# Kernel optimization log

Measured on AMD Instinct MI355X. Metric: run time of the kernel, lower is better.

## Reference

```python
import jax, jax.numpy as jnp
import numpy as np

L_LEVELS = 10
LEVEL_DIM = 4
BASE_RES = 16
T_HASH = 2 ** 21
DEG_VIEW = 4
DENSITY_BIAS = -1.0
RGB_PADDING = 0.001
RES = (BASE_RES * 2 ** np.arange(L_LEVELS)).astype(np.float32)  # 16..8192
CORNERS = np.array([[(i >> 2) & 1, (i >> 1) & 1, i & 1] for i in range(8)], np.int32)  # [8,3]
P1 = jnp.uint32(2654435761)
P2 = jnp.uint32(805459861)


def hash_grid_encode(pts, embeddings):
    """pts [N,3] in [-1,1]; embeddings [L,T,D] -> [N,L,D] trilinear hash-grid features."""
    x01 = (pts + 1.0) * 0.5  # [N,3] in [0,1]

    def level(emb, r):
        pos = x01 * r - 0.5  # align_corners=False style
        p0 = jnp.floor(pos)
        frac = pos - p0  # [N,3]
        coords = (p0.astype(jnp.int32)[:, None, :] + CORNERS).astype(jnp.uint32)  # [N,8,3]
        h = coords[..., 0] ^ (coords[..., 1] * P1) ^ (coords[..., 2] * P2)
        idx = (h & jnp.uint32(T_HASH - 1)).astype(jnp.int32)  # [N,8]
        w = jnp.prod(jnp.where(CORNERS == 1, frac[:, None, :], 1.0 - frac[:, None, :]), axis=-1)  # [N,8]
        vals = emb[idx]  # [N,8,D]
        return jnp.einsum('ncd,nc->nd', vals, w)

    feats = jax.vmap(level)(embeddings, jnp.asarray(RES))  # [L,N,D]
    return jnp.moveaxis(feats, 0, 1)  # [N,L,D]


def pos_enc(d, min_deg=0, max_deg=DEG_VIEW):
    scales = 2.0 ** jnp.arange(min_deg, max_deg, dtype=jnp.float32)
    xb = (d[..., None, :] * scales[:, None]).reshape(*d.shape[:-1], -1)  # [...,3*deg]
    four = jnp.sin(jnp.concatenate([xb, xb + 0.5 * jnp.pi], axis=-1))
    return jnp.concatenate([d, four], axis=-1)  # [..., 3 + 6*deg] = 27


def setup_inputs() -> dict:
    key = jax.random.key(0)
    ks = jax.random.split(key, 10)
    B, S, n = 1024, 32, 6
    means = jax.random.uniform(ks[0], (B, S, n, 3), minval=-1.0, maxval=1.0)
    stds = jax.random.uniform(ks[1], (B, S, n), minval=0.001, maxval=0.05)
    vd = jax.random.normal(ks[2], (B, 3))
    viewdirs = vd / jnp.linalg.norm(vd, axis=-1, keepdims=True)
    embeddings = jax.random.normal(ks[3], (L_LEVELS, T_HASH, LEVEL_DIM)) * 0.1

    def lin(k, i, o):
        return jax.random.normal(k, (i, o)) * (1.0 / np.sqrt(i))

    return {
        'rand': 0,
        'means': means, 'stds': stds, 'viewdirs': viewdirs, 'embeddings': embeddings,
        'Wd0': lin(ks[4], 40, 64), 'bd0': jnp.zeros(64),
        'Wd1': lin(ks[5], 64, 256), 'bd1': jnp.zeros(256),
        'Wv0': lin(ks[6], 283, 256), 'bv0': jnp.zeros(256),
        'Wv1': lin(ks[7], 539, 256), 'bv1': jnp.zeros(256),
        'Wr': lin(ks[8], 256, 3), 'br': jnp.zeros(3),
    }


def reference(rand, means, stds, viewdirs, embeddings, Wd0, bd0, Wd1, bd1,
              Wv0, bv0, Wv1, bv1, Wr, br):
    B, S, n = means.shape[:3]
    # --- predict_density ---
    feats = hash_grid_encode(means.reshape(-1, 3), embeddings)
    feats = feats.reshape(B, S, n, L_LEVELS, LEVEL_DIM)
    gs = jnp.asarray(RES)
    # erf re-weighting by per-level grid size (ZipNeRF anti-aliasing)
    w = jax.lax.erf(1.0 / jnp.clip(jnp.sqrt(8.0 * stds[..., None] ** 2 * gs ** 2), 1e-10))  # [B,S,n,L]
    feat = (feats * w[..., None]).mean(axis=-3).reshape(B, S, L_LEVELS * LEVEL_DIM)  # mean over multisamples n
    h = jax.nn.relu(feat @ Wd0 + bd0)
    x = h @ Wd1 + bd1  # [B,S,256] bottleneck
    density = jax.nn.softplus(x[..., 0] + DENSITY_BIAS)
    # --- view-dependent rgb branch ---
    dir_enc = pos_enc(viewdirs)  # [B,27]
    de = jnp.broadcast_to(dir_enc[:, None, :], (B, S, dir_enc.shape[-1]))
    x_in = jnp.concatenate([x, de], axis=-1)  # [B,S,283]
    h = jax.nn.relu(x_in @ Wv0 + bv0)
    h = jnp.concatenate([h, x_in], axis=-1)  # skip connection at layer 0 -> [B,S,539]
    h = jax.nn.relu(h @ Wv1 + bv1)
    rgb = jax.nn.sigmoid(h @ Wr + br)  # rgb_premultiplier=1, rgb_bias=0
    rgb = rgb * (1.0 + 2.0 * RGB_PADDING) - RGB_PADDING
    return density, rgb
```

## Files before the change

### kernel.cpp

```cpp
#include <hip/hip_runtime.h>

#define HASH_T    2097152u
#define HASH_MASK 2097151u
#define PRIME1 2654435761u
#define PRIME2 805459861u

typedef __attribute__((ext_vector_type(8))) short bf16x8;
typedef __attribute__((ext_vector_type(4))) float f32x4;
typedef __attribute__((ext_vector_type(4))) unsigned short us4;

__device__ __forceinline__ unsigned short bf16_hi(float x){
    unsigned u = __float_as_uint(x);
    return (unsigned short)((u + 0x7FFFu + ((u >> 16) & 1u)) >> 16);
}
__device__ __forceinline__ float bf16f(unsigned short h){
    return __uint_as_float((unsigned)h << 16);
}
__device__ __forceinline__ void split2(float x, unsigned short& h, unsigned short& l){
    h = bf16_hi(x);
    l = bf16_hi(x - bf16f(h));
}

__global__ __launch_bounds__(256) void pack_weights_kernel(
    const float* __restrict__ Wd0, const float* __restrict__ Wd1,
    const float* __restrict__ Wv0, const float* __restrict__ Wv1,
    unsigned short* __restrict__ pk)
{
    int tid = blockIdx.x * 256 + threadIdx.x;
    if (tid >= 424 * 512) return;
    int pair = tid >> 9;
    int li   = tid & 511;
    int lane = li >> 3, j = li & 7;
    int kq = ((lane >> 4) << 3) + j;
    int cl = lane & 15;
    float w;
    if (pair < 8) {
        int idx = pair; int kt = idx >> 2, ct = idx & 3;
        int k = kt * 32 + kq, c = ct * 16 + cl;
        w = (k < 40) ? Wd0[k * 64 + c] : 0.0f;
    } else if (pair < 40) {
        int idx = pair - 8; int kt = idx >> 4, ct = idx & 15;
        int k = kt * 32 + kq, c = ct * 16 + cl;
        w = Wd1[k * 256 + c];
    } else if (pair < 168) {
        int idx = pair - 40; int kt = idx >> 4, ct = idx & 15;
        int k = kt * 32 + kq, c = ct * 16 + cl;
        w = Wv0[k * 256 + c];
    } else {
        int idx = pair - 168;
        int kt = idx >> 4, ct = idx & 15;
        int k = kt * 32 + kq, c = ct * 16 + cl;
        int refr = (k < 256) ? (k + 256) : (k - 256);
        w = Wv1[refr * 256 + c];
    }
    unsigned short h, l; split2(w, h, l);
    pk[(size_t)pair * 1024 + li]       = h;
    pk[(size_t)pair * 1024 + 512 + li] = l;
}

__global__ __launch_bounds__(256) void hash_encode_kernel(
    const float* __restrict__ means, const float* __restrict__ stds,
    const float* __restrict__ emb, float* __restrict__ feat, int NS)
{
    int gid = blockIdx.x * 256 + threadIdx.x;
    if (gid >= NS * 10) return;
    int l = gid / NS;
    int s = gid - l * NS;
    float r = (float)(16 << l);
    const float* __restrict__ embL = emb + (size_t)l * (size_t)HASH_T * 4u;

    float a0 = 0.f, a1 = 0.f, a2 = 0.f, a3 = 0.f;
    #pragma unroll
    for (int n = 0; n < 6; ++n) {
        const float* mp = means + ((size_t)s * 6 + n) * 3;
        float sd = stds[(size_t)s * 6 + n];
        float px = (mp[0] + 1.0f) * 0.5f * r - 0.5f;
        float py = (mp[1] + 1.0f) * 0.5f * r - 0.5f;
        float pz = (mp[2] + 1.0f) * 0.5f * r - 0.5f;
        float fx = floorf(px), fy = floorf(py), fz = floorf(pz);
        float rx = px - fx, ry = py - fy, rz = pz - fz;
        int ix = (int)fx, iy = (int)fy, iz = (int)fz;
        unsigned hx[2] = { (unsigned)ix,          (unsigned)(ix + 1) };
        unsigned hy[2] = { (unsigned)iy * PRIME1, (unsigned)(iy + 1) * PRIME1 };
        unsigned hz[2] = { (unsigned)iz * PRIME2, (unsigned)(iz + 1) * PRIME2 };
        float wx[2] = { 1.0f - rx, rx };
        float wy[2] = { 1.0f - ry, ry };
        float wz[2] = { 1.0f - rz, rz };
        float t8 = 8.0f * (sd * sd) * (r * r);
        float wl = erff(1.0f / fmaxf(sqrtf(t8), 1e-10f));
        float v0 = 0.f, v1 = 0.f, v2 = 0.f, v3 = 0.f;
        #pragma unroll
        for (int c = 0; c < 8; ++c) {
            int bx = (c >> 2) & 1, by = (c >> 1) & 1, bz = c & 1;
            unsigned idx = (hx[bx] ^ hy[by] ^ hz[bz]) & HASH_MASK;
            const float4 e = *reinterpret_cast<const float4*>(embL + (size_t)idx * 4u);
            float w = wx[bx] * wy[by] * wz[bz];
            v0 += w * e.x; v1 += w * e.y; v2 += w * e.z; v3 += w * e.w;
        }
        a0 += wl * v0; a1 += wl * v1; a2 += wl * v2; a3 += wl * v3;
    }
    const float inv6 = 1.0f / 6.0f;
    float4 o; o.x = a0 * inv6; o.y = a1 * inv6; o.z = a2 * inv6; o.w = a3 * inv6;
    *reinterpret_cast<float4*>(feat + (size_t)s * 40 + l * 4) = o;
}

template<int KT, int NC>
__device__ __forceinline__ void gemm_layer(
    const unsigned short* __restrict__ pkBase, int NCT, int ct0, int kOff,
    const unsigned short (*Ahi)[584], const unsigned short (*Alo)[584],
    int lane, f32x4 acc[NC][2])
{
    const int r = lane & 15;
    const int kg = (lane >> 4) * 8;
    for (int kt = 0; kt < KT; ++kt) {
        const int ke = kOff + kt * 32 + kg;
        bf16x8 bh[2], bl[2];
        #pragma unroll
        for (int st = 0; st < 2; ++st) {
            bh[st] = *reinterpret_cast<const bf16x8*>(&Ahi[st * 16 + r][ke]);
            bl[st] = *reinterpret_cast<const bf16x8*>(&Alo[st * 16 + r][ke]);
        }
        #pragma unroll
        for (int ci = 0; ci < NC; ++ci) {
            const unsigned short* pf = pkBase + (size_t)(kt * NCT + ct0 + ci) * 1024 + lane * 8;
            bf16x8 ah = *reinterpret_cast<const bf16x8*>(pf);
            bf16x8 al = *reinterpret_cast<const bf16x8*>(pf + 512);
            #pragma unroll
            for (int st = 0; st < 2; ++st) {
                acc[ci][st] = __builtin_amdgcn_mfma_f32_16x16x32_bf16(ah, bh[st], acc[ci][st], 0, 0, 0);
                acc[ci][st] = __builtin_amdgcn_mfma_f32_16x16x32_bf16(ah, bl[st], acc[ci][st], 0, 0, 0);
                acc[ci][st] = __builtin_amdgcn_mfma_f32_16x16x32_bf16(al, bh[st], acc[ci][st], 0, 0, 0);
            }
        }
    }
}

template<int NC, bool RELU>
__device__ __forceinline__ void epilogue_store(
    f32x4 acc[NC][2], int ct0, int lane, const float* bias, int outOff,
    unsigned short (*Ahi)[584], unsigned short (*Alo)[584])
{
    const int r = lane & 15, g = lane >> 4;
    #pragma unroll
    for (int ci = 0; ci < NC; ++ci) {
        const int c0 = (ct0 + ci) * 16 + g * 4;
        const float4 bb = *reinterpret_cast<const float4*>(&bias[c0]);
        #pragma unroll
        for (int st = 0; st < 2; ++st) {
            const int s = st * 16 + r;
            float v[4] = { acc[ci][st][0] + bb.x, acc[ci][st][1] + bb.y,
                           acc[ci][st][2] + bb.z, acc[ci][st][3] + bb.w };
            us4 H, L;
            #pragma unroll
            for (int q = 0; q < 4; ++q) {
                float vv = RELU ? fmaxf(v[q], 0.0f) : v[q];
                unsigned short h, l; split2(vv, h, l);
                H[q] = h; L[q] = l;
            }
            *reinterpret_cast<us4*>(&Ahi[s][outOff + c0]) = H;
            *reinterpret_cast<us4*>(&Alo[s][outOff + c0]) = L;
        }
    }
}

__global__ __launch_bounds__(256, 2) void mlp_mfma_kernel(
    const float* __restrict__ feat, const float* __restrict__ vdirs,
    const unsigned short* __restrict__ pk,
    const float* __restrict__ bd0, const float* __restrict__ bd1,
    const float* __restrict__ Wv0, const float* __restrict__ bv0,
    const float* __restrict__ Wv1, const float* __restrict__ bv1,
    const float* __restrict__ Wr,  const float* __restrict__ br,
    float* __restrict__ outD, float* __restrict__ outRGB)
{
    __shared__ __align__(16) unsigned short sAhi[32][584];
    __shared__ __align__(16) unsigned short sAlo[32][584];
    __shared__ float sDe[32];
    __shared__ float sDv0[256];
    __shared__ float sDv1[256];
    __shared__ float sRed[32][8][3];

    const int t = threadIdx.x;
    const int lane = t & 63;
    const int w = t >> 6;
    const int b = blockIdx.x;
    const int base = b * 32;

    {
        int s = t >> 3, kg = t & 7;
        float v[8];
        if (kg < 5) {
            const float* fp = feat + (size_t)(base + s) * 40 + kg * 8;
            #pragma unroll
            for (int q = 0; q < 8; ++q) v[q] = fp[q];
        } else {
            #pragma unroll
            for (int q = 0; q < 8; ++q) v[q] = 0.0f;
        }
        us4 H0, H1, L0v, L1v;
        #pragma unroll
        for (int q = 0; q < 4; ++q) {
            unsigned short h, l;
            split2(v[q], h, l);       H0[q] = h; L0v[q] = l;
            split2(v[q + 4], h, l);   H1[q] = h; L1v[q] = l;
        }
        *reinterpret_cast<us4*>(&sAhi[s][kg * 8])     = H0;
        *reinterpret_cast<us4*>(&sAhi[s][kg * 8 + 4]) = H1;
        *reinterpret_cast<us4*>(&sAlo[s][kg * 8])     = L0v;
        *reinterpret_cast<us4*>(&sAlo[s][kg * 8 + 4]) = L1v;
    }
    if (t < 27) {
        float d0 = vdirs[b * 3 + 0], d1 = vdirs[b * 3 + 1], d2 = vdirs[b * 3 + 2];
        float val;
        if (t < 3) val = (t == 0) ? d0 : ((t == 1) ? d1 : d2);
        else {
            int u = t - 3, half = u / 12, jk = u % 12;
            int j = jk / 3, k = jk % 3;
            float dk = (k == 0) ? d0 : ((k == 1) ? d1 : d2);
            float xb = dk * (float)(1 << j);
            val = sinf(half ? (xb + 1.57079632679489662f) : xb);
        }
        sDe[t] = val;
    }
    __syncthreads();

    {
        int c = t;
        float a0 = bv0[c], a1 = bv1[c];
        #pragma unroll
        for (int k = 0; k < 27; ++k) {
            float dv = sDe[k];
            a0 += dv * Wv0[(256 + k) * 256 + c];
            a1 += dv * Wv1[(512 + k) * 256 + c];
        }
        sDv0[c] = a0; sDv1[c] = a1;
    }

    {
        f32x4 acc[1][2] = {};
        gemm_layer<2, 1>(pk, 4, w, 0, sAhi, sAlo, lane, acc);
        __syncthreads();
        epilogue_store<1, true>(acc, w, lane, bd0, 0, sAhi, sAlo);
    }
    __syncthreads();

    {
        f32x4 acc[4][2] = {};
        gemm_layer<2, 4>(pk + 8192, 16, w * 4, 0, sAhi, sAlo, lane, acc);
        if (w == 0 && (lane >> 4) == 0) {
            #pragma unroll
            for (int st = 0; st < 2; ++st) {
                float x0 = acc[0][st][0] + bd1[0];
                int s = st * 16 + (lane & 15);
                float vv = x0 - 1.0f;
                outD[base + s] = fmaxf(vv, 0.0f) + log1pf(expf(-fabsf(vv)));
            }
        }
        epilogue_store<4, false>(acc, w * 4, lane, bd1, 64, sAhi, sAlo);
    }
    __syncthreads();

    {
        f32x4 acc[4][2] = {};
        gemm_layer<8, 4>(pk + 40960, 16, w * 4, 64, sAhi, sAlo, lane, acc);
        epilogue_store<4, true>(acc, w * 4, lane, sDv0, 320, sAhi, sAlo);
    }
    __syncthreads();

    {
        f32x4 acc[4][2] = {};
        gemm_layer<16, 4>(pk + 172032, 16, w * 4, 64, sAhi, sAlo, lane, acc);
        __syncthreads();
        epilogue_store<4, true>(acc, w * 4, lane, sDv1, 0, sAhi, sAlo);
    }
    __syncthreads();

    {
        int s = t & 31, jj = t >> 5;
        float p0 = 0.f, p1 = 0.f, p2 = 0.f;
        int k0 = jj * 32;
        #pragma unroll 2
        for (int q = 0; q < 4; ++q) {
            us4 vh[2], vl[2];
            *reinterpret_cast<uint4*>(vh) = *reinterpret_cast<const uint4*>(&sAhi[s][k0 + q * 8]);
            *reinterpret_cast<uint4*>(vl) = *reinterpret_cast<const uint4*>(&sAlo[s][k0 + q * 8]);
            #pragma unroll
            for (int e = 0; e < 8; ++e) {
                int k = k0 + q * 8 + e;
                float hv = bf16f(((const unsigned short*)vh)[e]) + bf16f(((const unsigned short*)vl)[e]);
                p0 += hv * Wr[k * 3 + 0];
                p1 += hv * Wr[k * 3 + 1];
                p2 += hv * Wr[k * 3 + 2];
            }
        }
        sRed[s][jj][0] = p0; sRed[s][jj][1] = p1; sRed[s][jj][2] = p2;
    }
    __syncthreads();
    if (t < 96) {
        int s = t & 31, ch = t >> 5;
        float a = br[ch];
        #pragma unroll
        for (int j = 0; j < 8; ++j) a += sRed[s][j][ch];
        float sg = 1.0f / (1.0f + expf(-a));
        outRGB[(size_t)(base + s) * 3 + ch] = sg * 1.002f - 0.001f;
    }
}

extern "C" void kernel_launch(void* const* d_in, const int* in_sizes, int n_in,
                              void* d_out, int out_size, void* d_ws, size_t ws_size,
                              hipStream_t stream) {
    const float* means = (const float*)d_in[1];
    const float* stds_ = (const float*)d_in[2];
    const float* vdirs = (const float*)d_in[3];
    const float* emb   = (const float*)d_in[4];
    const float* Wd0 = (const float*)d_in[5];
    const float* bd0 = (const float*)d_in[6];
    const float* Wd1 = (const float*)d_in[7];
    const float* bd1 = (const float*)d_in[8];
    const float* Wv0 = (const float*)d_in[9];
    const float* bv0 = (const float*)d_in[10];
    const float* Wv1 = (const float*)d_in[11];
    const float* bv1 = (const float*)d_in[12];
    const float* Wr  = (const float*)d_in[13];
    const float* br  = (const float*)d_in[14];

    const int B  = in_sizes[3] / 3;
    const int NS = B * 32;

    float* feat = (float*)d_ws;
    unsigned short* pk = (unsigned short*)((char*)d_ws + (size_t)NS * 40 * 4);

    hipLaunchKernelGGL(pack_weights_kernel, dim3((424 * 512 + 255) / 256), dim3(256), 0, stream,
                       Wd0, Wd1, Wv0, Wv1, pk);

    int total = NS * 10;
    hipLaunchKernelGGL(hash_encode_kernel, dim3((total + 255) / 256), dim3(256), 0, stream,
                       means, stds_, emb, feat, NS);

    float* outD   = (float*)d_out;
    float* outRGB = outD + NS;
    hipLaunchKernelGGL(mlp_mfma_kernel, dim3(B), dim3(256), 0, stream,
                       feat, vdirs, pk, bd0, bd1, Wv0, bv0, Wv1, bv1, Wr, br,
                       outD, outRGB);
}
```

Measured before the change: 229.9 us.

## Remap hash encoding to wave-per-sample lanes and widen MLP tiles to 64 rows

The hash encoder now assigns one wavefront per group of samples, with each lane handling one multisample-corner pair and reducing across the wave with shuffles. Previously each thread walked all 48 gathers for one sample and level. The MLP kernel now processes 64 rows per 512-thread block and prefetches the next k-tile of packed weights into registers. It also vectorizes feature loads and replaces the shared-memory RGB reduction with shuffles. The goal is more memory-level parallelism in the gathers and more reuse of each weight fragment. The cost is more shuffle work per level, lanes left idle (n>=6), and higher register and LDS use per block.

```diff
diff --git a/kernel.cpp b/kernel.cpp
--- a/kernel.cpp
+++ b/kernel.cpp
@@ -58,95 +58,121 @@
     pk[(size_t)pair * 1024 + 512 + li] = l;
 }
 
-__global__ __launch_bounds__(256) void hash_encode_kernel(
+__global__ __launch_bounds__(256, 4) void hash_encode_wave(
     const float* __restrict__ means, const float* __restrict__ stds,
     const float* __restrict__ emb, float* __restrict__ feat, int NS)
 {
-    int gid = blockIdx.x * 256 + threadIdx.x;
-    if (gid >= NS * 10) return;
-    int l = gid / NS;
-    int s = gid - l * NS;
-    float r = (float)(16 << l);
-    const float* __restrict__ embL = emb + (size_t)l * (size_t)HASH_T * 4u;
-
-    float a0 = 0.f, a1 = 0.f, a2 = 0.f, a3 = 0.f;
-    #pragma unroll
-    for (int n = 0; n < 6; ++n) {
-        const float* mp = means + ((size_t)s * 6 + n) * 3;
-        float sd = stds[(size_t)s * 6 + n];
-        float px = (mp[0] + 1.0f) * 0.5f * r - 0.5f;
-        float py = (mp[1] + 1.0f) * 0.5f * r - 0.5f;
-        float pz = (mp[2] + 1.0f) * 0.5f * r - 0.5f;
-        float fx = floorf(px), fy = floorf(py), fz = floorf(pz);
-        float rx = px - fx, ry = py - fy, rz = pz - fz;
-        int ix = (int)fx, iy = (int)fy, iz = (int)fz;
-        unsigned hx[2] = { (unsigned)ix,          (unsigned)(ix + 1) };
-        unsigned hy[2] = { (unsigned)iy * PRIME1, (unsigned)(iy + 1) * PRIME1 };
-        unsigned hz[2] = { (unsigned)iz * PRIME2, (unsigned)(iz + 1) * PRIME2 };
-        float wx[2] = { 1.0f - rx, rx };
-        float wy[2] = { 1.0f - ry, ry };
-        float wz[2] = { 1.0f - rz, rz };
-        float t8 = 8.0f * (sd * sd) * (r * r);
-        float wl = erff(1.0f / fmaxf(sqrtf(t8), 1e-10f));
-        float v0 = 0.f, v1 = 0.f, v2 = 0.f, v3 = 0.f;
-        #pragma unroll
-        for (int c = 0; c < 8; ++c) {
-            int bx = (c >> 2) & 1, by = (c >> 1) & 1, bz = c & 1;
-            unsigned idx = (hx[bx] ^ hy[by] ^ hz[bz]) & HASH_MASK;
-            const float4 e = *reinterpret_cast<const float4*>(embL + (size_t)idx * 4u);
-            float w = wx[bx] * wy[by] * wz[bz];
-            v0 += w * e.x; v1 += w * e.y; v2 += w * e.z; v3 += w * e.w;
-        }
-        a0 += wl * v0; a1 += wl * v1; a2 += wl * v2; a3 += wl * v3;
-    }
+    const int lane = threadIdx.x & 63;
+    const int gwave = (blockIdx.x * 256 + threadIdx.x) >> 6;
+    const int n = lane >> 3;
+    const int c = lane & 7;
+    const int bx = (c >> 2) & 1, by = (c >> 1) & 1, bz = c & 1;
+    const bool act = (n < 6);
     const float inv6 = 1.0f / 6.0f;
-    float4 o; o.x = a0 * inv6; o.y = a1 * inv6; o.z = a2 * inv6; o.w = a3 * inv6;
-    *reinterpret_cast<float4*>(feat + (size_t)s * 40 + l * 4) = o;
+
+    int s0 = gwave * 4;
+    for (int si = 0; si < 4; ++si) {
+        int s = s0 + si;
+        if (s >= NS) return;
+        float mx = 0.f, my = 0.f, mz = 0.f, sd = 1.0f;
+        if (act) {
+            const float* mp = means + ((size_t)s * 6 + n) * 3;
+            mx = mp[0]; my = mp[1]; mz = mp[2];
+            sd = stds[(size_t)s * 6 + n];
+        }
+        float sd2_8 = 8.0f * sd * sd;
+        #pragma unroll 2
+        for (int l = 0; l < 10; ++l) {
+            float r = (float)(16 << l);
+            float px = (mx + 1.0f) * 0.5f * r - 0.5f;
+            float py = (my + 1.0f) * 0.5f * r - 0.5f;
+            float pz = (mz + 1.0f) * 0.5f * r - 0.5f;
+            float fx = floorf(px), fy = floorf(py), fz = floorf(pz);
+            float rx = px - fx, ry = py - fy, rz = pz - fz;
+            int ix = (int)fx + bx, iy = (int)fy + by, iz = (int)fz + bz;
+            unsigned h = (unsigned)ix ^ ((unsigned)iy * PRIME1) ^ ((unsigned)iz * PRIME2);
+            unsigned idx = h & HASH_MASK;
+            float wx = bx ? rx : 1.0f - rx;
+            float wy = by ? ry : 1.0f - ry;
+            float wz = bz ? rz : 1.0f - rz;
+            float wl = erff(1.0f / fmaxf(sqrtf(sd2_8 * r * r), 1e-10f));
+            float w = act ? (wx * wy * wz) * wl : 0.0f;
+            const float4 e = *reinterpret_cast<const float4*>(
+                emb + ((size_t)l * HASH_T + idx) * 4u);
+            float a0 = w * e.x, a1 = w * e.y, a2 = w * e.z, a3 = w * e.w;
+            #pragma unroll
+            for (int m = 1; m < 64; m <<= 1) {
+                a0 += __shfl_xor(a0, m);
+                a1 += __shfl_xor(a1, m);
+                a2 += __shfl_xor(a2, m);
+                a3 += __shfl_xor(a3, m);
+            }
+            if (lane == 0) {
+                float4 o; o.x = a0 * inv6; o.y = a1 * inv6; o.z = a2 * inv6; o.w = a3 * inv6;
+                *reinterpret_cast<float4*>(feat + (size_t)s * 40 + l * 4) = o;
+            }
+        }
+    }
 }
 
 template<int KT, int NC>
-__device__ __forceinline__ void gemm_layer(
+__device__ __forceinline__ void gemm64(
     const unsigned short* __restrict__ pkBase, int NCT, int ct0, int kOff,
     const unsigned short (*Ahi)[584], const unsigned short (*Alo)[584],
-    int lane, f32x4 acc[NC][2])
+    int lane, f32x4 acc[NC][4])
 {
     const int r = lane & 15;
     const int kg = (lane >> 4) * 8;
+    bf16x8 ah[NC], al[NC];
+    #pragma unroll
+    for (int ci = 0; ci < NC; ++ci) {
+        const unsigned short* pf = pkBase + (size_t)(ct0 + ci) * 1024 + (size_t)lane * 8;
+        ah[ci] = *reinterpret_cast<const bf16x8*>(pf);
+        al[ci] = *reinterpret_cast<const bf16x8*>(pf + 512);
+    }
+    #pragma unroll
     for (int kt = 0; kt < KT; ++kt) {
+        bf16x8 ahn[NC], aln[NC];
+        if (kt + 1 < KT) {
+            #pragma unroll
+            for (int ci = 0; ci < NC; ++ci) {
+                const unsigned short* pf = pkBase
+                    + (size_t)((kt + 1) * NCT + ct0 + ci) * 1024 + (size_t)lane * 8;
+                ahn[ci] = *reinterpret_cast<const bf16x8*>(pf);
+                aln[ci] = *reinterpret_cast<const bf16x8*>(pf + 512);
+            }
+        }
         const int ke = kOff + kt * 32 + kg;
-        bf16x8 bh[2], bl[2];
-        #pragma unroll
-        for (int st = 0; st < 2; ++st) {
-            bh[st] = *reinterpret_cast<const bf16x8*>(&Ahi[st * 16 + r][ke]);
-            bl[st] = *reinterpret_cast<const bf16x8*>(&Alo[st * 16 + r][ke]);
-        }
-        #pragma unroll
-        for (int ci = 0; ci < NC; ++ci) {
-            const unsigned short* pf = pkBase + (size_t)(kt * NCT + ct0 + ci) * 1024 + lane * 8;
-            bf16x8 ah = *reinterpret_cast<const bf16x8*>(pf);
-            bf16x8 al = *reinterpret_cast<const bf16x8*>(pf + 512);
-            #pragma unroll
-            for (int st = 0; st < 2; ++st) {
-                acc[ci][st] = __builtin_amdgcn_mfma_f32_16x16x32_bf16(ah, bh[st], acc[ci][st], 0, 0, 0);
-                acc[ci][st] = __builtin_amdgcn_mfma_f32_16x16x32_bf16(ah, bl[st], acc[ci][st], 0, 0, 0);
-                acc[ci][st] = __builtin_amdgcn_mfma_f32_16x16x32_bf16(al, bh[st], acc[ci][st], 0, 0, 0);
-            }
-        }
+        #pragma unroll
+        for (int st = 0; st < 4; ++st) {
+            bf16x8 bh = *reinterpret_cast<const bf16x8*>(&Ahi[st * 16 + r][ke]);
+            bf16x8 bl = *reinterpret_cast<const bf16x8*>(&Alo[st * 16 + r][ke]);
+            #pragma unroll
+            for (int ci = 0; ci < NC; ++ci) {
+                acc[ci][st] = __builtin_amdgcn_mfma_f32_16x16x32_bf16(ah[ci], bh, acc[ci][st], 0, 0, 0);
+                acc[ci][st] = __builtin_amdgcn_mfma_f32_16x16x32_bf16(ah[ci], bl, acc[ci][st], 0, 0, 0);
+                acc[ci][st] = __builtin_amdgcn_mfma_f32_16x16x32_bf16(al[ci], bh, acc[ci][st], 0, 0, 0);
+            }
+        }
+        #pragma unroll
+        for (int ci = 0; ci < NC; ++ci) { ah[ci] = ahn[ci]; al[ci] = aln[ci]; }
     }
 }
 
 template<int NC, bool RELU>
-__device__ __forceinline__ void epilogue_store(
-    f32x4 acc[NC][2], int ct0, int lane, const float* bias, int outOff,
+__device__ __forceinline__ void epi64(
+    f32x4 acc[NC][4], int ct0, int lane,
+    const float* biasA, const float* biasB, int outOff,
     unsigned short (*Ahi)[584], unsigned short (*Alo)[584])
 {
     const int r = lane & 15, g = lane >> 4;
     #pragma unroll
     for (int ci = 0; ci < NC; ++ci) {
         const int c0 = (ct0 + ci) * 16 + g * 4;
-        const float4 bb = *reinterpret_cast<const float4*>(&bias[c0]);
-        #pragma unroll
-        for (int st = 0; st < 2; ++st) {
+        #pragma unroll
+        for (int st = 0; st < 4; ++st) {
+            const float* bp = (st < 2) ? biasA : biasB;
+            const float4 bb = *reinterpret_cast<const float4*>(&bp[c0]);
             const int s = st * 16 + r;
             float v[4] = { acc[ci][st][0] + bb.x, acc[ci][st][1] + bb.y,
                            acc[ci][st][2] + bb.z, acc[ci][st][3] + bb.w };
@@ -163,7 +189,7 @@
     }
 }
 
-__global__ __launch_bounds__(256, 2) void mlp_mfma_kernel(
+__global__ __launch_bounds__(512, 2) void mlp_mfma_kernel(
     const float* __restrict__ feat, const float* __restrict__ vdirs,
     const unsigned short* __restrict__ pk,
     const float* __restrict__ bd0, const float* __restrict__ bd1,
@@ -172,26 +198,26 @@
     const float* __restrict__ Wr,  const float* __restrict__ br,
     float* __restrict__ outD, float* __restrict__ outRGB)
 {
-    __shared__ __align__(16) unsigned short sAhi[32][584];
-    __shared__ __align__(16) unsigned short sAlo[32][584];
-    __shared__ float sDe[32];
-    __shared__ float sDv0[256];
-    __shared__ float sDv1[256];
-    __shared__ float sRed[32][8][3];
+    __shared__ __align__(16) unsigned short sAhi[64][584];
+    __shared__ __align__(16) unsigned short sAlo[64][584];
+    __shared__ float sDe[2][32];
+    __shared__ float sDv0[2][256];
+    __shared__ float sDv1[2][256];
 
     const int t = threadIdx.x;
     const int lane = t & 63;
     const int w = t >> 6;
     const int b = blockIdx.x;
-    const int base = b * 32;
+    const int base = b * 64;
 
     {
         int s = t >> 3, kg = t & 7;
         float v[8];
         if (kg < 5) {
-            const float* fp = feat + (size_t)(base + s) * 40 + kg * 8;
-            #pragma unroll
-            for (int q = 0; q < 8; ++q) v[q] = fp[q];
+            const float4 f0 = *reinterpret_cast<const float4*>(feat + (size_t)(base + s) * 40 + kg * 8);
+            const float4 f1 = *reinterpret_cast<const float4*>(feat + (size_t)(base + s) * 40 + kg * 8 + 4);
+            v[0]=f0.x; v[1]=f0.y; v[2]=f0.z; v[3]=f0.w;
+            v[4]=f1.x; v[5]=f1.y; v[6]=f1.z; v[7]=f1.w;
         } else {
             #pragma unroll
             for (int q = 0; q < 8; ++q) v[q] = 0.0f;
@@ -208,76 +234,79 @@
         *reinterpret_cast<us4*>(&sAlo[s][kg * 8])     = L0v;
         *reinterpret_cast<us4*>(&sAlo[s][kg * 8 + 4]) = L1v;
     }
-    if (t < 27) {
-        float d0 = vdirs[b * 3 + 0], d1 = vdirs[b * 3 + 1], d2 = vdirs[b * 3 + 2];
+    if (t < 54) {
+        int ry = (t >= 27) ? 1 : 0;
+        int u = t - ry * 27;
+        float d0 = vdirs[(2 * b + ry) * 3 + 0];
+        float d1 = vdirs[(2 * b + ry) * 3 + 1];
+        float d2 = vdirs[(2 * b + ry) * 3 + 2];
         float val;
-        if (t < 3) val = (t == 0) ? d0 : ((t == 1) ? d1 : d2);
+        if (u < 3) val = (u == 0) ? d0 : ((u == 1) ? d1 : d2);
         else {
-            int u = t - 3, half = u / 12, jk = u % 12;
+            int v2 = u - 3, half = v2 / 12, jk = v2 % 12;
             int j = jk / 3, k = jk % 3;
             float dk = (k == 0) ? d0 : ((k == 1) ? d1 : d2);
             float xb = dk * (float)(1 << j);
             val = sinf(half ? (xb + 1.57079632679489662f) : xb);
         }
-        sDe[t] = val;
-    }
-    __syncthreads();
-
-    {
-        int c = t;
+        sDe[ry][u] = val;
+    }
+    __syncthreads();
+
+    {
+        int c = t & 255, ry = t >> 8;
         float a0 = bv0[c], a1 = bv1[c];
         #pragma unroll
         for (int k = 0; k < 27; ++k) {
-            float dv = sDe[k];
+            float dv = sDe[ry][k];
             a0 += dv * Wv0[(256 + k) * 256 + c];
             a1 += dv * Wv1[(512 + k) * 256 + c];
         }
-        sDv0[c] = a0; sDv1[c] = a1;
-    }
-
-    {
-        f32x4 acc[1][2] = {};
-        gemm_layer<2, 1>(pk, 4, w, 0, sAhi, sAlo, lane, acc);
+        sDv0[ry][c] = a0; sDv1[ry][c] = a1;
+    }
+
+    {
+        f32x4 acc[1][4] = {};
+        if (w < 4) gemm64<2, 1>(pk, 4, w, 0, sAhi, sAlo, lane, acc);
         __syncthreads();
-        epilogue_store<1, true>(acc, w, lane, bd0, 0, sAhi, sAlo);
-    }
-    __syncthreads();
-
-    {
-        f32x4 acc[4][2] = {};
-        gemm_layer<2, 4>(pk + 8192, 16, w * 4, 0, sAhi, sAlo, lane, acc);
+        if (w < 4) epi64<1, true>(acc, w, lane, bd0, bd0, 0, sAhi, sAlo);
+    }
+    __syncthreads();
+
+    {
+        f32x4 acc[2][4] = {};
+        gemm64<2, 2>(pk + 8192, 16, w * 2, 0, sAhi, sAlo, lane, acc);
         if (w == 0 && (lane >> 4) == 0) {
             #pragma unroll
-            for (int st = 0; st < 2; ++st) {
+            for (int st = 0; st < 4; ++st) {
                 float x0 = acc[0][st][0] + bd1[0];
                 int s = st * 16 + (lane & 15);
                 float vv = x0 - 1.0f;
                 outD[base + s] = fmaxf(vv, 0.0f) + log1pf(expf(-fabsf(vv)));
             }
         }
-        epilogue_store<4, false>(acc, w * 4, lane, bd1, 64, sAhi, sAlo);
-    }
-    __syncthreads();
-
-    {
-        f32x4 acc[4][2] = {};
-        gemm_layer<8, 4>(pk + 40960, 16, w * 4, 64, sAhi, sAlo, lane, acc);
-        epilogue_store<4, true>(acc, w * 4, lane, sDv0, 320, sAhi, sAlo);
-    }
-    __syncthreads();
-
-    {
-        f32x4 acc[4][2] = {};
-        gemm_layer<16, 4>(pk + 172032, 16, w * 4, 64, sAhi, sAlo, lane, acc);
+        epi64<2, false>(acc, w * 2, lane, bd1, bd1, 64, sAhi, sAlo);
+    }
+    __syncthreads();
+
+    {
+        f32x4 acc[2][4] = {};
+        gemm64<8, 2>(pk + 40960, 16, w * 2, 64, sAhi, sAlo, lane, acc);
+        epi64<2, true>(acc, w * 2, lane, sDv0[0], sDv0[1], 320, sAhi, sAlo);
+    }
+    __syncthreads();
+
+    {
+        f32x4 acc[2][4] = {};
+        gemm64<16, 2>(pk + 172032, 16, w * 2, 64, sAhi, sAlo, lane, acc);
         __syncthreads();
-        epilogue_store<4, true>(acc, w * 4, lane, sDv1, 0, sAhi, sAlo);
-    }
-    __syncthreads();
-
-    {
-        int s = t & 31, jj = t >> 5;
+        epi64<2, true>(acc, w * 2, lane, sDv1[0], sDv1[1], 0, sAhi, sAlo);
+    }
+    __syncthreads();
+
+    {
+        int s = t >> 3, j = t & 7, k0 = j * 32;
         float p0 = 0.f, p1 = 0.f, p2 = 0.f;
-        int k0 = jj * 32;
         #pragma unroll 2
         for (int q = 0; q < 4; ++q) {
             us4 vh[2], vl[2];
@@ -292,16 +321,17 @@
                 p2 += hv * Wr[k * 3 + 2];
             }
         }
-        sRed[s][jj][0] = p0; sRed[s][jj][1] = p1; sRed[s][jj][2] = p2;
-    }
-    __syncthreads();
-    if (t < 96) {
-        int s = t & 31, ch = t >> 5;
-        float a = br[ch];
-        #pragma unroll
-        for (int j = 0; j < 8; ++j) a += sRed[s][j][ch];
-        float sg = 1.0f / (1.0f + expf(-a));
-        outRGB[(size_t)(base + s) * 3 + ch] = sg * 1.002f - 0.001f;
+        #pragma unroll
+        for (int m = 1; m < 8; m <<= 1) {
+            p0 += __shfl_xor(p0, m);
+            p1 += __shfl_xor(p1, m);
+            p2 += __shfl_xor(p2, m);
+        }
+        if (j < 3) {
+            float a = ((j == 0) ? p0 : (j == 1) ? p1 : p2) + br[j];
+            float sg = 1.0f / (1.0f + expf(-a));
+            outRGB[(size_t)(base + s) * 3 + j] = sg * 1.002f - 0.001f;
+        }
     }
 }
 
@@ -332,13 +362,13 @@
     hipLaunchKernelGGL(pack_weights_kernel, dim3((424 * 512 + 255) / 256), dim3(256), 0, stream,
                        Wd0, Wd1, Wv0, Wv1, pk);
 
-    int total = NS * 10;
-    hipLaunchKernelGGL(hash_encode_kernel, dim3((total + 255) / 256), dim3(256), 0, stream,
+    int nwaves = (NS + 3) / 4;
+    hipLaunchKernelGGL(hash_encode_wave, dim3((nwaves * 64 + 255) / 256), dim3(256), 0, stream,
                        means, stds_, emb, feat, NS);
 
     float* outD   = (float*)d_out;
     float* outRGB = outD + NS;
-    hipLaunchKernelGGL(mlp_mfma_kernel, dim3(B), dim3(256), 0, stream,
+    hipLaunchKernelGGL(mlp_mfma_kernel, dim3(NS / 64), dim3(512), 0, stream,
                        feat, vdirs, pk, bd0, bd1, Wv0, bv0, Wv1, bv1, Wr, br,
                        outD, outRGB);
 }
```

Result: faster. 209.2 us (-9.0%).
